# Optimization experiments

Hardware: AMD Instinct MI355X
Metric: run time of the kernel (lower is better)

Reference implementation:

```python
import jax, jax.numpy as jnp
import numpy as np

D = 32        # number of TT cores (d)
R = 16        # tt_rank
B = 262144    # batch size


def setup_inputs() -> dict:
    key = jax.random.key(0)
    k1, k2, k3, k4 = jax.random.split(key, 4)
    return {
        "X": jax.random.randint(k1, (B, D), 0, 2, dtype=jnp.int32),
        "core_first": jax.random.normal(k2, (1, R, 2), dtype=jnp.float32),
        "cores_mid": jax.random.normal(k3, (D - 2, R, R, 2), dtype=jnp.float32),
        "core_last": jax.random.normal(k4, (R, 1, 2), dtype=jnp.float32),
    }


def reference(X, core_first, cores_mid, core_last):
    # First core: cores[0][:, :, X[:,0]] -> [1, R, B] -> permute -> [B, 1, R].
    # We carry the squeezed [B, R] row vector instead of [B, 1, R].
    carry0 = jnp.take(core_first[0], X[:, 0], axis=-1).T  # [B, R]

    def step(carry, inp):
        core, idx = inp                       # core: [R, R, 2], idx: [B]
        c = jnp.take(core, idx, axis=2)       # gathered core: [R, R, B]
        new = jnp.einsum('br,rsb->bs', carry, c)  # batched (1xR)@(RxR)
        return new, None

    # Middle cores i = 1 .. D-2 (sequential chain, data-dependent).
    carry, _ = jax.lax.scan(step, carry0, (cores_mid, X[:, 1:D - 1].T))

    # Last core: cores[-1][:, :, X[:,-1]] -> [R, 1, B]; contract to scalar per batch.
    c_last = jnp.take(core_last[:, 0, :], X[:, -1], axis=-1)  # [R, B]
    out = jnp.einsum('br,rb->b', carry, c_last)               # [B]  (squeeze of [B,1,1])
    return out
```

## Files before the change

kernel.cpp:

```cpp
#include <hip/hip_runtime.h>


#define R 16
#define TT_D 32
#define BATCH 262144

#define OFF_V8   0
#define OFF_P8   (OFF_V8 + 4096)
#define OFF_Q8   (OFF_P8 + 65536)
#define OFF_W8   (OFF_Q8 + 65536)
#define OFF_V16  (OFF_W8 + 4096)
#define OFF_W16  (OFF_V16 + 1048576)
#define WS_FLOATS (OFF_W16 + 1048576)

typedef int   v4i __attribute__((ext_vector_type(4)));
typedef float v4f __attribute__((ext_vector_type(4)));
typedef float v2f __attribute__((ext_vector_type(2)));

__global__ __launch_bounds__(256) void tt_byte_build(const float* __restrict__ cf,
                                                     const float* __restrict__ cm,
                                                     const float* __restrict__ cl,
                                                     float* __restrict__ ws) {
    __shared__ float sA[256], sB[256];
    const int g = blockIdx.x;
    const int t = threadIdx.x;

    if (g < 512) {
        const bool isP = (g < 256);
        const int e = g & 255;
        const int base = isP ? 7 : 15;
        const int r = t >> 4, s = t & 15;
        {
            const int b = (e >> 7) & 1;
            sA[t] = cm[(((base * 16 + r) * 16) + s) * 2 + b];
        }
        float* cur = sA; float* nxt = sB;
        float acc = 0.f;
        for (int j = 1; j < 8; j++) {
            __syncthreads();
            const int b = (e >> (7 - j)) & 1;
            const float* M = cm + (base + j) * 512 + b;
            acc = 0.f;
            #pragma unroll
            for (int k = 0; k < 16; k++)
                acc += cur[r * 16 + k] * M[(k * 16 + s) * 2];
            nxt[t] = acc;
            float* tmp = cur; cur = nxt; nxt = tmp;
        }
        ws[(isP ? OFF_P8 : OFF_Q8) + (e << 8) + t] = acc;
    } else if (g < 528) {
        const int eb = (g - 512) * 16;
        const int el = t >> 4, s = t & 15;
        const int e = eb + el;
        sA[t] = cf[s * 2 + ((e >> 7) & 1)];
        float* cur = sA; float* nxt = sB;
        float acc = 0.f;
        for (int j = 0; j < 7; j++) {
            __syncthreads();
            const int b = (e >> (6 - j)) & 1;
            const float* M = cm + j * 512 + b;
            acc = 0.f;
            #pragma unroll
            for (int r2 = 0; r2 < 16; r2++)
                acc += cur[el * 16 + r2] * M[(r2 * 16 + s) * 2];
            nxt[t] = acc;
            float* tmp = cur; cur = nxt; nxt = tmp;
        }
        ws[OFF_V8 + eb * 16 + t] = acc;
    } else {
        const int eb = (g - 528) * 16;
        const int el = t >> 4, r = t & 15;
        const int e = eb + el;
        sA[t] = cl[r * 2 + (e & 1)];
        float* cur = sA; float* nxt = sB;
        float acc = 0.f;
        for (int j = 0; j < 7; j++) {
            __syncthreads();
            const int c = 29 - j;
            const int b = (e >> (1 + j)) & 1;
            const float* M = cm + c * 512 + b;
            acc = 0.f;
            #pragma unroll
            for (int k = 0; k < 16; k++)
                acc += M[(r * 16 + k) * 2] * cur[el * 16 + k];
            nxt[t] = acc;
            float* tmp = cur; cur = nxt; nxt = tmp;
        }
        ws[OFF_W8 + eb * 16 + t] = acc;
    }
}

__global__ __launch_bounds__(256) void tt_tab(float* __restrict__ ws) {
    const int t = threadIdx.x;
    if (blockIdx.x < 256) {
        const int l = blockIdx.x;
        __shared__ float sP[256];
        sP[t] = ws[OFF_P8 + (l << 8) + t];
        __syncthreads();
        const int h = t;
        const float* v8 = ws + OFF_V8 + (h << 4);
        float v[16];
        #pragma unroll
        for (int k = 0; k < 16; k++) v[k] = v8[k];
        float o[16];
        #pragma unroll
        for (int s = 0; s < 16; s++) o[s] = 0.f;
        #pragma unroll
        for (int r = 0; r < 16; r++) {
            const float a = v[r];
            #pragma unroll
            for (int s = 0; s < 16; s++) o[s] += a * sP[r * 16 + s];
        }
        float* dst = ws + OFF_V16 + ((size_t)((h << 8) | l) << 4);
        #pragma unroll
        for (int s = 0; s < 16; s++) dst[s] = o[s];
    } else {
        const int h = blockIdx.x - 256;
        __shared__ float sQ[256];
        sQ[t] = ws[OFF_Q8 + (h << 8) + t];
        __syncthreads();
        const int l = t;
        const float* w8 = ws + OFF_W8 + (l << 4);
        float w[16];
        #pragma unroll
        for (int k = 0; k < 16; k++) w[k] = w8[k];
        float o[16];
        #pragma unroll
        for (int r = 0; r < 16; r++) {
            float acc = 0.f;
            #pragma unroll
            for (int k = 0; k < 16; k++) acc += sQ[r * 16 + k] * w[k];
            o[r] = acc;
        }
        float* dst = ws + OFF_W16 + ((size_t)((h << 8) | l) << 4);
        #pragma unroll
        for (int r = 0; r < 16; r++) dst[r] = o[r];
    }
}

__global__ __launch_bounds__(256) void tt_main2(const int* __restrict__ X,
                                                const float* __restrict__ ws,
                                                float* __restrict__ out) {
    const int tid = blockIdx.x * 256 + threadIdx.x;
    const v4i* Xr = (const v4i*)(X + (size_t)tid * 64);
    v4i c[16];
    #pragma unroll
    for (int q = 0; q < 16; q++) c[q] = __builtin_nontemporal_load(Xr + q);

    unsigned key[4] = { 0u, 0u, 0u, 0u };
    #pragma unroll
    for (int q = 0; q < 16; q++) {
        const unsigned nib = ((unsigned)(c[q].x & 1) << 3) | ((unsigned)(c[q].y & 1) << 2) |
                             ((unsigned)(c[q].z & 1) << 1) | (unsigned)(c[q].w & 1);
        key[q >> 2] = (key[q >> 2] << 4) | nib;
    }

    const v4f* v0 = (const v4f*)(ws + OFF_V16 + (size_t)key[0] * 16);
    const v4f* w0 = (const v4f*)(ws + OFF_W16 + (size_t)key[1] * 16);
    const v4f* v1 = (const v4f*)(ws + OFF_V16 + (size_t)key[2] * 16);
    const v4f* w1 = (const v4f*)(ws + OFF_W16 + (size_t)key[3] * 16);

    v4f acc0 = { 0.f, 0.f, 0.f, 0.f }, acc1 = { 0.f, 0.f, 0.f, 0.f };
    #pragma unroll
    for (int k = 0; k < 4; k++) acc0 += v0[k] * w0[k];
    #pragma unroll
    for (int k = 0; k < 4; k++) acc1 += v1[k] * w1[k];

    v2f res;
    res.x = acc0.x + acc0.y + acc0.z + acc0.w;
    res.y = acc1.x + acc1.y + acc1.z + acc1.w;
    __builtin_nontemporal_store(res, (v2f*)(out + (size_t)tid * 2));
}

__global__ __launch_bounds__(256) void tt_direct(const int* __restrict__ X,
                                                 const float* __restrict__ cf,
                                                 const float* __restrict__ cm,
                                                 const float* __restrict__ cl,
                                                 float* __restrict__ out) {
    __shared__ float scm[30 * 16 * 16 * 2];
    for (int i = threadIdx.x; i < 30 * 16 * 16 * 2; i += blockDim.x) scm[i] = cm[i];
    __syncthreads();
    const int b = blockIdx.x * blockDim.x + threadIdx.x;
    if (b >= BATCH) return;
    const int* xr = X + (size_t)b * TT_D;
    float v[R], nv[R];
    const int x0 = xr[0] & 1;
    #pragma unroll
    for (int r = 0; r < R; r++) v[r] = cf[r * 2 + x0];
    for (int i = 1; i <= 30; i++) {
        const int bit = xr[i] & 1;
        const float* M = scm + (i - 1) * 512;
        #pragma unroll
        for (int s2 = 0; s2 < R; s2++) {
            float acc = 0.f;
            #pragma unroll
            for (int r = 0; r < R; r++) acc += v[r] * M[(r * 16 + s2) * 2 + bit];
            nv[s2] = acc;
        }
        #pragma unroll
        for (int s2 = 0; s2 < R; s2++) v[s2] = nv[s2];
    }
    const int xl = xr[31] & 1;
    float acc = 0.f;
    #pragma unroll
    for (int r = 0; r < R; r++) acc += v[r] * cl[r * 2 + xl];
    out[b] = acc;
}

extern "C" void kernel_launch(void* const* d_in, const int* in_sizes, int n_in,
                              void* d_out, int out_size, void* d_ws, size_t ws_size,
                              hipStream_t stream) {
    const int* X = (const int*)d_in[0];
    const float* cf = (const float*)d_in[1];
    const float* cm = (const float*)d_in[2];
    const float* cl = (const float*)d_in[3];
    float* out = (float*)d_out;

    if (ws_size >= (size_t)WS_FLOATS * sizeof(float)) {
        float* ws = (float*)d_ws;
        tt_byte_build<<<544, 256, 0, stream>>>(cf, cm, cl, ws);
        tt_tab<<<512, 256, 0, stream>>>(ws);
        tt_main2<<<BATCH / 512, 256, 0, stream>>>(X, ws, out);
    } else {
        tt_direct<<<(BATCH + 255) / 256, 256, 0, stream>>>(X, cf, cm, cl, out);
    }
}
```

Measured before the change: 129.2 us.

## Fuse build, table and lookup kernels into one persistent kernel with grid barriers

Merges the three-kernel pipeline (byte-chain build, 16-bit table build, per-row lookup) into a single 512-block kernel separated by software grid barriers built on an atomic counter and generation word in the workspace. The V8/W8 builds now run on 32 of the existing blocks instead of 32 extra blocks. This removes two kernel launch boundaries and their gaps, but adds a memset launch for the barrier words and relies on all 512 blocks being co-resident. On mi355x with 256 CUs and launch bounds allowing two blocks per CU, co-residency is plausible.

```diff
diff --git a/kernel.cpp b/kernel.cpp
--- a/kernel.cpp
+++ b/kernel.cpp
@@ -4,6 +4,7 @@
 #define R 16
 #define TT_D 32
 #define BATCH 262144
+#define NBLK 512
 
 #define OFF_V8   0
 #define OFF_P8   (OFF_V8 + 4096)
@@ -11,31 +12,51 @@
 #define OFF_W8   (OFF_Q8 + 65536)
 #define OFF_V16  (OFF_W8 + 4096)
 #define OFF_W16  (OFF_V16 + 1048576)
-#define WS_FLOATS (OFF_W16 + 1048576)
+#define OFF_BAR  (OFF_W16 + 1048576)
+#define WS_FLOATS (OFF_BAR + 16)
 
 typedef int   v4i __attribute__((ext_vector_type(4)));
 typedef float v4f __attribute__((ext_vector_type(4)));
 typedef float v2f __attribute__((ext_vector_type(2)));
 
-__global__ __launch_bounds__(256) void tt_byte_build(const float* __restrict__ cf,
-                                                     const float* __restrict__ cm,
-                                                     const float* __restrict__ cl,
-                                                     float* __restrict__ ws) {
+__device__ __forceinline__ void grid_barrier(unsigned* cnt, unsigned* gen) {
+    __syncthreads();
+    if (threadIdx.x == 0) {
+        __threadfence();
+        const unsigned g0 = __hip_atomic_load(gen, __ATOMIC_RELAXED, __HIP_MEMORY_SCOPE_AGENT);
+        const unsigned prev = __hip_atomic_fetch_add(cnt, 1u, __ATOMIC_ACQ_REL, __HIP_MEMORY_SCOPE_AGENT);
+        if (prev == (unsigned)(NBLK - 1)) {
+            __hip_atomic_store(cnt, 0u, __ATOMIC_RELAXED, __HIP_MEMORY_SCOPE_AGENT);
+            __hip_atomic_fetch_add(gen, 1u, __ATOMIC_ACQ_REL, __HIP_MEMORY_SCOPE_AGENT);
+        } else {
+            while (__hip_atomic_load(gen, __ATOMIC_ACQUIRE, __HIP_MEMORY_SCOPE_AGENT) == g0) {
+                __builtin_amdgcn_s_sleep(8);
+            }
+        }
+        __threadfence();
+    }
+    __syncthreads();
+}
+
+__global__ __launch_bounds__(256, 2) void tt_all(const int* __restrict__ X,
+                                                 const float* __restrict__ cf,
+                                                 const float* __restrict__ cm,
+                                                 const float* __restrict__ cl,
+                                                 float* __restrict__ ws,
+                                                 float* __restrict__ out) {
     __shared__ float sA[256], sB[256];
     const int g = blockIdx.x;
     const int t = threadIdx.x;
-
-    if (g < 512) {
+    unsigned* bar = (unsigned*)(ws + OFF_BAR);
+
+    {
         const bool isP = (g < 256);
         const int e = g & 255;
         const int base = isP ? 7 : 15;
         const int r = t >> 4, s = t & 15;
-        {
-            const int b = (e >> 7) & 1;
-            sA[t] = cm[(((base * 16 + r) * 16) + s) * 2 + b];
-        }
+        float acc = 0.f;
+        sA[t] = cm[base * 512 + r * 32 + s * 2 + ((e >> 7) & 1)];
         float* cur = sA; float* nxt = sB;
-        float acc = 0.f;
         for (int j = 1; j < 8; j++) {
             __syncthreads();
             const int b = (e >> (7 - j)) & 1;
@@ -43,59 +64,59 @@
             acc = 0.f;
             #pragma unroll
             for (int k = 0; k < 16; k++)
-                acc += cur[r * 16 + k] * M[(k * 16 + s) * 2];
+                acc += cur[r * 16 + k] * M[k * 32 + s * 2];
             nxt[t] = acc;
             float* tmp = cur; cur = nxt; nxt = tmp;
         }
         ws[(isP ? OFF_P8 : OFF_Q8) + (e << 8) + t] = acc;
-    } else if (g < 528) {
-        const int eb = (g - 512) * 16;
-        const int el = t >> 4, s = t & 15;
-        const int e = eb + el;
-        sA[t] = cf[s * 2 + ((e >> 7) & 1)];
-        float* cur = sA; float* nxt = sB;
-        float acc = 0.f;
-        for (int j = 0; j < 7; j++) {
+
+        if (isP && e < 16) {
             __syncthreads();
-            const int b = (e >> (6 - j)) & 1;
-            const float* M = cm + j * 512 + b;
-            acc = 0.f;
-            #pragma unroll
-            for (int r2 = 0; r2 < 16; r2++)
-                acc += cur[el * 16 + r2] * M[(r2 * 16 + s) * 2];
-            nxt[t] = acc;
-            float* tmp = cur; cur = nxt; nxt = tmp;
-        }
-        ws[OFF_V8 + eb * 16 + t] = acc;
-    } else {
-        const int eb = (g - 528) * 16;
-        const int el = t >> 4, r = t & 15;
-        const int e = eb + el;
-        sA[t] = cl[r * 2 + (e & 1)];
-        float* cur = sA; float* nxt = sB;
-        float acc = 0.f;
-        for (int j = 0; j < 7; j++) {
+            const int el = t >> 4, sv = t & 15;
+            const int E = e * 16 + el;
+            float a2 = 0.f;
+            sA[t] = cf[sv * 2 + ((E >> 7) & 1)];
+            cur = sA; nxt = sB;
+            for (int j = 0; j < 7; j++) {
+                __syncthreads();
+                const int b = (E >> (6 - j)) & 1;
+                const float* M = cm + j * 512 + b;
+                a2 = 0.f;
+                #pragma unroll
+                for (int r2 = 0; r2 < 16; r2++)
+                    a2 += cur[el * 16 + r2] * M[r2 * 32 + sv * 2];
+                nxt[t] = a2;
+                float* tmp = cur; cur = nxt; nxt = tmp;
+            }
+            ws[OFF_V8 + e * 256 + t] = a2;
+        } else if (!isP && e < 16) {
             __syncthreads();
-            const int c = 29 - j;
-            const int b = (e >> (1 + j)) & 1;
-            const float* M = cm + c * 512 + b;
-            acc = 0.f;
-            #pragma unroll
-            for (int k = 0; k < 16; k++)
-                acc += M[(r * 16 + k) * 2] * cur[el * 16 + k];
-            nxt[t] = acc;
-            float* tmp = cur; cur = nxt; nxt = tmp;
-        }
-        ws[OFF_W8 + eb * 16 + t] = acc;
-    }
-}
-
-__global__ __launch_bounds__(256) void tt_tab(float* __restrict__ ws) {
-    const int t = threadIdx.x;
-    if (blockIdx.x < 256) {
-        const int l = blockIdx.x;
-        __shared__ float sP[256];
-        sP[t] = ws[OFF_P8 + (l << 8) + t];
+            const int el = t >> 4, rv = t & 15;
+            const int E = e * 16 + el;
+            float a2 = 0.f;
+            sA[t] = cl[rv * 2 + (E & 1)];
+            cur = sA; nxt = sB;
+            for (int j = 0; j < 7; j++) {
+                __syncthreads();
+                const int c = 29 - j;
+                const int b = (E >> (1 + j)) & 1;
+                const float* M = cm + c * 512 + b;
+                a2 = 0.f;
+                #pragma unroll
+                for (int k = 0; k < 16; k++)
+                    a2 += M[rv * 32 + k * 2] * cur[el * 16 + k];
+                nxt[t] = a2;
+                float* tmp = cur; cur = nxt; nxt = tmp;
+            }
+            ws[OFF_W8 + e * 256 + t] = a2;
+        }
+    }
+
+    grid_barrier(bar, bar + 1);
+
+    if (g < 256) {
+        const int l = g;
+        sA[t] = ws[OFF_P8 + (l << 8) + t];
         __syncthreads();
         const int h = t;
         const float* v8 = ws + OFF_V8 + (h << 4);
@@ -109,15 +130,14 @@
         for (int r = 0; r < 16; r++) {
             const float a = v[r];
             #pragma unroll
-            for (int s = 0; s < 16; s++) o[s] += a * sP[r * 16 + s];
+            for (int s = 0; s < 16; s++) o[s] += a * sA[r * 16 + s];
         }
         float* dst = ws + OFF_V16 + ((size_t)((h << 8) | l) << 4);
         #pragma unroll
         for (int s = 0; s < 16; s++) dst[s] = o[s];
     } else {
-        const int h = blockIdx.x - 256;
-        __shared__ float sQ[256];
-        sQ[t] = ws[OFF_Q8 + (h << 8) + t];
+        const int h = g - 256;
+        sA[t] = ws[OFF_Q8 + (h << 8) + t];
         __syncthreads();
         const int l = t;
         const float* w8 = ws + OFF_W8 + (l << 4);
@@ -129,47 +149,47 @@
         for (int r = 0; r < 16; r++) {
             float acc = 0.f;
             #pragma unroll
-            for (int k = 0; k < 16; k++) acc += sQ[r * 16 + k] * w[k];
+            for (int k = 0; k < 16; k++) acc += sA[r * 16 + k] * w[k];
             o[r] = acc;
         }
         float* dst = ws + OFF_W16 + ((size_t)((h << 8) | l) << 4);
         #pragma unroll
         for (int r = 0; r < 16; r++) dst[r] = o[r];
     }
-}
-
-__global__ __launch_bounds__(256) void tt_main2(const int* __restrict__ X,
-                                                const float* __restrict__ ws,
-                                                float* __restrict__ out) {
-    const int tid = blockIdx.x * 256 + threadIdx.x;
-    const v4i* Xr = (const v4i*)(X + (size_t)tid * 64);
-    v4i c[16];
-    #pragma unroll
-    for (int q = 0; q < 16; q++) c[q] = __builtin_nontemporal_load(Xr + q);
-
-    unsigned key[4] = { 0u, 0u, 0u, 0u };
-    #pragma unroll
-    for (int q = 0; q < 16; q++) {
-        const unsigned nib = ((unsigned)(c[q].x & 1) << 3) | ((unsigned)(c[q].y & 1) << 2) |
-                             ((unsigned)(c[q].z & 1) << 1) | (unsigned)(c[q].w & 1);
-        key[q >> 2] = (key[q >> 2] << 4) | nib;
-    }
-
-    const v4f* v0 = (const v4f*)(ws + OFF_V16 + (size_t)key[0] * 16);
-    const v4f* w0 = (const v4f*)(ws + OFF_W16 + (size_t)key[1] * 16);
-    const v4f* v1 = (const v4f*)(ws + OFF_V16 + (size_t)key[2] * 16);
-    const v4f* w1 = (const v4f*)(ws + OFF_W16 + (size_t)key[3] * 16);
-
-    v4f acc0 = { 0.f, 0.f, 0.f, 0.f }, acc1 = { 0.f, 0.f, 0.f, 0.f };
-    #pragma unroll
-    for (int k = 0; k < 4; k++) acc0 += v0[k] * w0[k];
-    #pragma unroll
-    for (int k = 0; k < 4; k++) acc1 += v1[k] * w1[k];
-
-    v2f res;
-    res.x = acc0.x + acc0.y + acc0.z + acc0.w;
-    res.y = acc1.x + acc1.y + acc1.z + acc1.w;
-    __builtin_nontemporal_store(res, (v2f*)(out + (size_t)tid * 2));
+
+    grid_barrier(bar, bar + 1);
+
+    {
+        const int tid = g * 256 + t;
+        const v4i* Xr = (const v4i*)(X + (size_t)tid * 64);
+        v4i c[16];
+        #pragma unroll
+        for (int q = 0; q < 16; q++) c[q] = __builtin_nontemporal_load(Xr + q);
+
+        unsigned key[4] = { 0u, 0u, 0u, 0u };
+        #pragma unroll
+        for (int q = 0; q < 16; q++) {
+            const unsigned nib = ((unsigned)(c[q].x & 1) << 3) | ((unsigned)(c[q].y & 1) << 2) |
+                                 ((unsigned)(c[q].z & 1) << 1) | (unsigned)(c[q].w & 1);
+            key[q >> 2] = (key[q >> 2] << 4) | nib;
+        }
+
+        const v4f* v0 = (const v4f*)(ws + OFF_V16 + (size_t)key[0] * 16);
+        const v4f* w0 = (const v4f*)(ws + OFF_W16 + (size_t)key[1] * 16);
+        const v4f* v1 = (const v4f*)(ws + OFF_V16 + (size_t)key[2] * 16);
+        const v4f* w1 = (const v4f*)(ws + OFF_W16 + (size_t)key[3] * 16);
+
+        v4f acc0 = { 0.f, 0.f, 0.f, 0.f }, acc1 = { 0.f, 0.f, 0.f, 0.f };
+        #pragma unroll
+        for (int k = 0; k < 4; k++) acc0 += v0[k] * w0[k];
+        #pragma unroll
+        for (int k = 0; k < 4; k++) acc1 += v1[k] * w1[k];
+
+        v2f res;
+        res.x = acc0.x + acc0.y + acc0.z + acc0.w;
+        res.y = acc1.x + acc1.y + acc1.z + acc1.w;
+        __builtin_nontemporal_store(res, (v2f*)(out + (size_t)tid * 2));
+    }
 }
 
 __global__ __launch_bounds__(256) void tt_direct(const int* __restrict__ X,
@@ -218,9 +238,8 @@
 
     if (ws_size >= (size_t)WS_FLOATS * sizeof(float)) {
         float* ws = (float*)d_ws;
-        tt_byte_build<<<544, 256, 0, stream>>>(cf, cm, cl, ws);
-        tt_tab<<<512, 256, 0, stream>>>(ws);
-        tt_main2<<<BATCH / 512, 256, 0, stream>>>(X, ws, out);
+        hipMemsetAsync((void*)(ws + OFF_BAR), 0, 64, stream);
+        tt_all<<<NBLK, 256, 0, stream>>>(X, cf, cm, cl, ws, out);
     } else {
         tt_direct<<<(BATCH + 255) / 256, 256, 0, stream>>>(X, cf, cm, cl, out);
     }
```

After: 310.2 us. +140.2%, slower.

## Fuse byte-table build and 16-bit table expansion into one kernel

Applied to the files above, without the earlier changes.

Merges the two precompute kernels into a single tt_build kernel. Each block stages the relevant cores in shared memory with transposed layouts, computes its 8-core product matrix, and then expands its 16-bit prefix/suffix table rows in-thread, so intermediate tables no longer round-trip through global memory and one launch is dropped. The gather kernel now uses one thread per batch row instead of two, with a remapped V16 index. This adds redundant per-block recomputation of the 7-core chains and raises shared-memory use per block.

```diff
diff --git a/kernel.cpp b/kernel.cpp
--- a/kernel.cpp
+++ b/kernel.cpp
@@ -5,171 +5,169 @@
 #define TT_D 32
 #define BATCH 262144
 
-#define OFF_V8   0
-#define OFF_P8   (OFF_V8 + 4096)
-#define OFF_Q8   (OFF_P8 + 65536)
-#define OFF_W8   (OFF_Q8 + 65536)
-#define OFF_V16  (OFF_W8 + 4096)
-#define OFF_W16  (OFF_V16 + 1048576)
-#define WS_FLOATS (OFF_W16 + 1048576)
+#define OFF_V16  0
+#define OFF_W16  1048576
+#define WS_FLOATS 2097152
 
 typedef int   v4i __attribute__((ext_vector_type(4)));
 typedef float v4f __attribute__((ext_vector_type(4)));
-typedef float v2f __attribute__((ext_vector_type(2)));
-
-__global__ __launch_bounds__(256) void tt_byte_build(const float* __restrict__ cf,
-                                                     const float* __restrict__ cm,
-                                                     const float* __restrict__ cl,
-                                                     float* __restrict__ ws) {
-    __shared__ float sA[256], sB[256];
+
+#define L_TM   0
+#define L_TC   4096
+#define L_PING 7680
+#define L_PONG 7936
+#define L_PQT  8192
+#define L_CV   8448
+#define L_TOT  8480
+
+__global__ __launch_bounds__(256) void tt_build(const float* __restrict__ cf,
+                                                const float* __restrict__ cm,
+                                                const float* __restrict__ cl,
+                                                float* __restrict__ ws) {
+    __shared__ float sh[L_TOT];
     const int g = blockIdx.x;
     const int t = threadIdx.x;
-
-    if (g < 512) {
-        const bool isP = (g < 256);
-        const int e = g & 255;
-        const int base = isP ? 7 : 15;
+    const bool isV = (g < 256);
+    const int sel = isV ? g : (g - 256);
+
+    {
+        const float* src = cm + (isV ? 7 : 15) * 512;
+        for (int i = t; i < 4096; i += 256) {
+            const int c = i >> 9, j = i & 511;
+            const int r = j >> 5, s = (j >> 1) & 15, x = j & 1;
+            sh[L_TM + (((c << 1) + x) << 8) + (s << 4) + r] = src[i];
+        }
+    }
+    {
+        const float* src = cm + (isV ? 0 : 23) * 512;
+        for (int i = t; i < 3584; i += 256) {
+            const int c = i >> 9, j = i & 511;
+            const int r = j >> 5, s = (j >> 1) & 15, x = j & 1;
+            const int dst = isV ? ((s << 4) + r) : ((r << 4) + s);
+            sh[L_TC + (((c << 1) + x) << 8) + dst] = src[i];
+        }
+    }
+    if (t < 32) sh[L_CV + t] = isV ? cf[t] : cl[t];
+    __syncthreads();
+
+    {
         const int r = t >> 4, s = t & 15;
-        {
-            const int b = (e >> 7) & 1;
-            sA[t] = cm[(((base * 16 + r) * 16) + s) * 2 + b];
-        }
-        float* cur = sA; float* nxt = sB;
-        float acc = 0.f;
+        float acc = sh[L_TM + (((sel >> 7) & 1) << 8) + (s << 4) + r];
+        float* cur = sh + L_PING;
+        float* nxt = sh + L_PONG;
+        cur[t] = acc;
         for (int j = 1; j < 8; j++) {
             __syncthreads();
-            const int b = (e >> (7 - j)) & 1;
-            const float* M = cm + (base + j) * 512 + b;
+            const int bb = (sel >> (7 - j)) & 1;
+            const float* M = sh + L_TM + (((j << 1) + bb) << 8) + (s << 4);
+            const float* cr = cur + (r << 4);
             acc = 0.f;
             #pragma unroll
-            for (int k = 0; k < 16; k++)
-                acc += cur[r * 16 + k] * M[(k * 16 + s) * 2];
+            for (int k = 0; k < 16; k++) acc += cr[k] * M[k];
             nxt[t] = acc;
             float* tmp = cur; cur = nxt; nxt = tmp;
         }
-        ws[(isP ? OFF_P8 : OFF_Q8) + (e << 8) + t] = acc;
-    } else if (g < 528) {
-        const int eb = (g - 512) * 16;
-        const int el = t >> 4, s = t & 15;
-        const int e = eb + el;
-        sA[t] = cf[s * 2 + ((e >> 7) & 1)];
-        float* cur = sA; float* nxt = sB;
-        float acc = 0.f;
+        sh[L_PQT + (isV ? ((s << 4) + r) : (r << 4) + s)] = acc;
+    }
+    __syncthreads();
+
+    if (isV) {
+        const int h = t;
+        float v[16], nv[16];
+        const int b0 = (h >> 7) & 1;
+        #pragma unroll
+        for (int s = 0; s < 16; s++) v[s] = sh[L_CV + s * 2 + b0];
         for (int j = 0; j < 7; j++) {
-            __syncthreads();
-            const int b = (e >> (6 - j)) & 1;
-            const float* M = cm + j * 512 + b;
-            acc = 0.f;
-            #pragma unroll
-            for (int r2 = 0; r2 < 16; r2++)
-                acc += cur[el * 16 + r2] * M[(r2 * 16 + s) * 2];
-            nxt[t] = acc;
-            float* tmp = cur; cur = nxt; nxt = tmp;
-        }
-        ws[OFF_V8 + eb * 16 + t] = acc;
-    } else {
-        const int eb = (g - 528) * 16;
-        const int el = t >> 4, r = t & 15;
-        const int e = eb + el;
-        sA[t] = cl[r * 2 + (e & 1)];
-        float* cur = sA; float* nxt = sB;
-        float acc = 0.f;
-        for (int j = 0; j < 7; j++) {
-            __syncthreads();
-            const int c = 29 - j;
-            const int b = (e >> (1 + j)) & 1;
-            const float* M = cm + c * 512 + b;
-            acc = 0.f;
-            #pragma unroll
-            for (int k = 0; k < 16; k++)
-                acc += M[(r * 16 + k) * 2] * cur[el * 16 + k];
-            nxt[t] = acc;
-            float* tmp = cur; cur = nxt; nxt = tmp;
-        }
-        ws[OFF_W8 + eb * 16 + t] = acc;
-    }
-}
-
-__global__ __launch_bounds__(256) void tt_tab(float* __restrict__ ws) {
-    const int t = threadIdx.x;
-    if (blockIdx.x < 256) {
-        const int l = blockIdx.x;
-        __shared__ float sP[256];
-        sP[t] = ws[OFF_P8 + (l << 8) + t];
-        __syncthreads();
-        const int h = t;
-        const float* v8 = ws + OFF_V8 + (h << 4);
-        float v[16];
-        #pragma unroll
-        for (int k = 0; k < 16; k++) v[k] = v8[k];
+            const int bb = (h >> (6 - j)) & 1;
+            const float* Tj = sh + L_TC + (((j << 1) + bb) << 8);
+            #pragma unroll
+            for (int s = 0; s < 16; s++) {
+                const float* col = Tj + (s << 4);
+                float a = 0.f;
+                #pragma unroll
+                for (int r = 0; r < 16; r++) a += v[r] * col[r];
+                nv[s] = a;
+            }
+            #pragma unroll
+            for (int s = 0; s < 16; s++) v[s] = nv[s];
+        }
         float o[16];
         #pragma unroll
-        for (int s = 0; s < 16; s++) o[s] = 0.f;
-        #pragma unroll
-        for (int r = 0; r < 16; r++) {
-            const float a = v[r];
-            #pragma unroll
-            for (int s = 0; s < 16; s++) o[s] += a * sP[r * 16 + s];
-        }
-        float* dst = ws + OFF_V16 + ((size_t)((h << 8) | l) << 4);
+        for (int s = 0; s < 16; s++) {
+            const float* col = sh + L_PQT + (s << 4);
+            float a = 0.f;
+            #pragma unroll
+            for (int r = 0; r < 16; r++) a += v[r] * col[r];
+            o[s] = a;
+        }
+        float* dst = ws + OFF_V16 + ((size_t)((sel << 8) | h) << 4);
         #pragma unroll
         for (int s = 0; s < 16; s++) dst[s] = o[s];
     } else {
-        const int h = blockIdx.x - 256;
-        __shared__ float sQ[256];
-        sQ[t] = ws[OFF_Q8 + (h << 8) + t];
-        __syncthreads();
         const int l = t;
-        const float* w8 = ws + OFF_W8 + (l << 4);
-        float w[16];
-        #pragma unroll
-        for (int k = 0; k < 16; k++) w[k] = w8[k];
+        float w[16], nw[16];
+        const int bl = l & 1;
+        #pragma unroll
+        for (int r = 0; r < 16; r++) w[r] = sh[L_CV + r * 2 + bl];
+        for (int j = 0; j < 7; j++) {
+            const int cc = 6 - j;
+            const int bb = (l >> (1 + j)) & 1;
+            const float* Tj = sh + L_TC + (((cc << 1) + bb) << 8);
+            #pragma unroll
+            for (int r = 0; r < 16; r++) {
+                const float* row = Tj + (r << 4);
+                float a = 0.f;
+                #pragma unroll
+                for (int k = 0; k < 16; k++) a += row[k] * w[k];
+                nw[r] = a;
+            }
+            #pragma unroll
+            for (int r = 0; r < 16; r++) w[r] = nw[r];
+        }
         float o[16];
         #pragma unroll
         for (int r = 0; r < 16; r++) {
-            float acc = 0.f;
-            #pragma unroll
-            for (int k = 0; k < 16; k++) acc += sQ[r * 16 + k] * w[k];
-            o[r] = acc;
-        }
-        float* dst = ws + OFF_W16 + ((size_t)((h << 8) | l) << 4);
+            const float* row = sh + L_PQT + (r << 4);
+            float a = 0.f;
+            #pragma unroll
+            for (int k = 0; k < 16; k++) a += row[k] * w[k];
+            o[r] = a;
+        }
+        float* dst = ws + OFF_W16 + ((size_t)((sel << 8) | l) << 4);
         #pragma unroll
         for (int r = 0; r < 16; r++) dst[r] = o[r];
     }
 }
 
-__global__ __launch_bounds__(256) void tt_main2(const int* __restrict__ X,
-                                                const float* __restrict__ ws,
-                                                float* __restrict__ out) {
-    const int tid = blockIdx.x * 256 + threadIdx.x;
-    const v4i* Xr = (const v4i*)(X + (size_t)tid * 64);
-    v4i c[16];
-    #pragma unroll
-    for (int q = 0; q < 16; q++) c[q] = __builtin_nontemporal_load(Xr + q);
-
-    unsigned key[4] = { 0u, 0u, 0u, 0u };
-    #pragma unroll
-    for (int q = 0; q < 16; q++) {
-        const unsigned nib = ((unsigned)(c[q].x & 1) << 3) | ((unsigned)(c[q].y & 1) << 2) |
-                             ((unsigned)(c[q].z & 1) << 1) | (unsigned)(c[q].w & 1);
-        key[q >> 2] = (key[q >> 2] << 4) | nib;
-    }
-
-    const v4f* v0 = (const v4f*)(ws + OFF_V16 + (size_t)key[0] * 16);
-    const v4f* w0 = (const v4f*)(ws + OFF_W16 + (size_t)key[1] * 16);
-    const v4f* v1 = (const v4f*)(ws + OFF_V16 + (size_t)key[2] * 16);
-    const v4f* w1 = (const v4f*)(ws + OFF_W16 + (size_t)key[3] * 16);
-
-    v4f acc0 = { 0.f, 0.f, 0.f, 0.f }, acc1 = { 0.f, 0.f, 0.f, 0.f };
-    #pragma unroll
-    for (int k = 0; k < 4; k++) acc0 += v0[k] * w0[k];
-    #pragma unroll
-    for (int k = 0; k < 4; k++) acc1 += v1[k] * w1[k];
-
-    v2f res;
-    res.x = acc0.x + acc0.y + acc0.z + acc0.w;
-    res.y = acc1.x + acc1.y + acc1.z + acc1.w;
-    __builtin_nontemporal_store(res, (v2f*)(out + (size_t)tid * 2));
+__global__ __launch_bounds__(256) void tt_gather(const int* __restrict__ X,
+                                                 const float* __restrict__ ws,
+                                                 float* __restrict__ out) {
+    const int b = blockIdx.x * 256 + threadIdx.x;
+    const v4i* Xr = (const v4i*)(X + (size_t)b * TT_D);
+    v4i c[8];
+    #pragma unroll
+    for (int q = 0; q < 8; q++) c[q] = __builtin_nontemporal_load(Xr + q);
+
+    unsigned p = 0, s = 0;
+    #pragma unroll
+    for (int q = 0; q < 4; q++) {
+        p = (p << 4) | ((unsigned)(c[q].x & 1) << 3) | ((unsigned)(c[q].y & 1) << 2) |
+            ((unsigned)(c[q].z & 1) << 1) | (unsigned)(c[q].w & 1);
+    }
+    #pragma unroll
+    for (int q = 4; q < 8; q++) {
+        s = (s << 4) | ((unsigned)(c[q].x & 1) << 3) | ((unsigned)(c[q].y & 1) << 2) |
+            ((unsigned)(c[q].z & 1) << 1) | (unsigned)(c[q].w & 1);
+    }
+
+    const unsigned vi = ((p & 255u) << 8) | (p >> 8);
+    const v4f* v = (const v4f*)(ws + OFF_V16 + (size_t)vi * 16);
+    const v4f* w = (const v4f*)(ws + OFF_W16 + (size_t)s * 16);
+
+    v4f acc = { 0.f, 0.f, 0.f, 0.f };
+    #pragma unroll
+    for (int k = 0; k < 4; k++) acc += v[k] * w[k];
+    __builtin_nontemporal_store(acc.x + acc.y + acc.z + acc.w, out + b);
 }
 
 __global__ __launch_bounds__(256) void tt_direct(const int* __restrict__ X,
@@ -218,9 +216,8 @@
 
     if (ws_size >= (size_t)WS_FLOATS * sizeof(float)) {
         float* ws = (float*)d_ws;
-        tt_byte_build<<<544, 256, 0, stream>>>(cf, cm, cl, ws);
-        tt_tab<<<512, 256, 0, stream>>>(ws);
-        tt_main2<<<BATCH / 512, 256, 0, stream>>>(X, ws, out);
+        tt_build<<<512, 256, 0, stream>>>(cf, cm, cl, ws);
+        tt_gather<<<1024, 256, 0, stream>>>(X, ws, out);
     } else {
         tt_direct<<<(BATCH + 255) / 256, 256, 0, stream>>>(X, cf, cm, cl, out);
     }
```

Measured after the change: 123.3 us. 4.5% less time.
